# Performance work log

Measured on AMD Instinct MI355X. Metric: run time of the kernel, lower is better.

## Reference

```python
import jax, jax.numpy as jnp
import numpy as np

DIM = 192
HEADS = 6
HD = DIM // HEADS          # head dim = 32
WIN = 7
K = WIN * WIN              # 49 window positions
B, H, W = 4, 56, 56
EPS = 1e-5                 # BatchNorm2d eps
PAD = WIN // 2


def setup_inputs() -> dict:
    key = jax.random.key(0)
    ks = jax.random.split(key, 8)
    def n(k, shape, scale=0.02):
        return jax.random.normal(k, shape, dtype=jnp.float32) * scale
    return {
        "x": jax.random.normal(ks[0], (B, DIM, H, W), dtype=jnp.float32),
        "bn_gamma": jnp.ones((DIM,), jnp.float32),
        "bn_beta": jnp.zeros((DIM,), jnp.float32),
        "qkv_w": n(ks[1], (3 * DIM, DIM)),          # 1x1 conv as matmul
        "qkv_b": jnp.zeros((3 * DIM,), jnp.float32),
        "dm_w": n(ks[2], (K, 2 * HD, WIN, WIN)),    # convDotMul OIHW
        "dm_b": jnp.zeros((K,), jnp.float32),
        "rel_bias": n(ks[3], (K, HEADS)),           # relative_position_bias_table
        "proj_w": n(ks[4], (DIM, DIM)),
        "proj_b": jnp.zeros((DIM,), jnp.float32),
        "c1_w": n(ks[5], (4 * DIM, DIM)),
        "c1_b": jnp.zeros((4 * DIM,), jnp.float32),
        "c2_w": n(ks[6], (DIM, 4 * DIM)),
        "c2_b": jnp.zeros((DIM,), jnp.float32),
    }


def _conv1x1(x, w, b):
    # x: (B,C,H,W), w: (O,C) -> (B,O,H,W)
    return jnp.einsum('bchw,oc->bohw', x, w) + b[None, :, None, None]


def reference(x, bn_gamma, bn_beta, qkv_w, qkv_b, dm_w, dm_b, rel_bias,
              proj_w, proj_b, c1_w, c1_b, c2_w, c2_b):
    Bx, C, Hx, Wx = x.shape
    shortcut = x
    # BatchNorm2d (training-mode batch statistics, biased variance)
    mean = jnp.mean(x, axis=(0, 2, 3), keepdims=True)
    var = jnp.var(x, axis=(0, 2, 3), keepdims=True)
    xn = (x - mean) * jax.lax.rsqrt(var + EPS)
    xn = xn * bn_gamma[None, :, None, None] + bn_beta[None, :, None, None]
    # qkv: 1x1 conv -> (B,3,heads,hd,H,W)
    qkv = _conv1x1(xn, qkv_w, qkv_b).reshape(Bx, 3, HEADS, HD, Hx, Wx)
    q, k, v = qkv[:, 0], qkv[:, 1], qkv[:, 2]
    scale = HD ** (-0.5)
    # convDotMul on concat(q*scale, k) over merged (B*heads) batch
    qk = jnp.concatenate([(q * scale).reshape(Bx * HEADS, HD, Hx, Wx),
                          k.reshape(Bx * HEADS, HD, Hx, Wx)], axis=1)
    attn = jax.lax.conv_general_dilated(
        qk, dm_w, (1, 1), [(PAD, PAD), (PAD, PAD)],
        dimension_numbers=('NCHW', 'OIHW', 'NCHW')) + dm_b[None, :, None, None]
    attn = attn.reshape(Bx, HEADS, K, Hx, Wx)
    attn = attn + rel_bias.T[None, :, :, None, None]   # (1,heads,K,1,1)
    attn = jax.nn.softmax(attn, axis=2)
    # gather 49 zero-padded shifted views of v via patch extraction
    # channels of patches are (hd, kh*kw) row-major == torch loop i//7, i%7
    patches = jax.lax.conv_general_dilated_patches(
        v.reshape(Bx * HEADS, HD, Hx, Wx), (WIN, WIN), (1, 1),
        [(PAD, PAD), (PAD, PAD)], dimension_numbers=('NCHW', 'OIHW', 'NCHW'))
    patches = patches.reshape(Bx, HEADS, HD, K, Hx, Wx)
    out = jnp.einsum('bnckhw,bnkhw->bnchw', patches, attn).reshape(Bx, C, Hx, Wx)
    out = _conv1x1(out, proj_w, proj_b)
    x1 = shortcut + out
    # convLayers MLP (1x1 convs, exact GELU)
    h = _conv1x1(x1, c1_w, c1_b)
    h = jax.nn.gelu(h, approximate=False)
    h = _conv1x1(h, c2_w, c2_b)
    return x1 + h
```

## Files before the change

### kernel.cpp

```cpp
#include <hip/hip_runtime.h>
#include <hip/hip_bf16.h>
#include <math.h>

#define CDIM 192
#define NHEADS 6
#define WIN 7
#define KWIN 49
#define BATCH 4
#define PIX 3136
#define NPIX 12544
#define NIMG 24
#define EPSV 1e-5f

typedef __bf16 bf16x8 __attribute__((ext_vector_type(8)));
typedef float f32x16 __attribute__((ext_vector_type(16)));
typedef unsigned int uint4v __attribute__((ext_vector_type(4)));
typedef unsigned int uint2v __attribute__((ext_vector_type(2)));
typedef int int4x __attribute__((ext_vector_type(4)));
typedef int int8x __attribute__((ext_vector_type(8)));
typedef unsigned short u16;
typedef unsigned char u8;

__device__ inline u8 f32_to_fp8(float v) {
  return (u8)(__builtin_amdgcn_cvt_pk_fp8_f32(v, 0.f, 0, false) & 0xFF);
}

__device__ inline uint2v bf8_to_fp8x8(uint4v v) {
  const u16* h = (const u16*)&v;
  float f[8];
#pragma unroll
  for (int e = 0; e < 8; e++) {
    unsigned u = ((unsigned)h[e]) << 16;
    f[e] = __builtin_bit_cast(float, u);
  }
  int lo = __builtin_amdgcn_cvt_pk_fp8_f32(f[0], f[1], 0, false);
  lo = __builtin_amdgcn_cvt_pk_fp8_f32(f[2], f[3], lo, true);
  int hi = __builtin_amdgcn_cvt_pk_fp8_f32(f[4], f[5], 0, false);
  hi = __builtin_amdgcn_cvt_pk_fp8_f32(f[6], f[7], hi, true);
  uint2v r = {(unsigned)lo, (unsigned)hi};
  return r;
}

__global__ __launch_bounds__(256) void bn_stats_k(const float* __restrict__ x,
                                                  float* __restrict__ stats) {
  int c = blockIdx.x;
  float s = 0.f, q = 0.f;
  for (int n = threadIdx.x; n < BATCH * PIX; n += 256) {
    int b = n / PIX, p = n - b * PIX;
    float v = x[((size_t)b * CDIM + c) * PIX + p];
    s += v; q += v * v;
  }
  __shared__ float rs[256], rq[256];
  rs[threadIdx.x] = s; rq[threadIdx.x] = q;
  __syncthreads();
  for (int st = 128; st > 0; st >>= 1) {
    if (threadIdx.x < st) { rs[threadIdx.x] += rs[threadIdx.x + st]; rq[threadIdx.x] += rq[threadIdx.x + st]; }
    __syncthreads();
  }
  if (threadIdx.x == 0) {
    float mean = rs[0] / (float)(BATCH * PIX);
    float var = rq[0] / (float)(BATCH * PIX) - mean * mean;
    stats[c] = mean;
    stats[CDIM + c] = rsqrtf(var + EPSV);
  }
}

__device__ inline void pack_one(const float* __restrict__ W, u16* __restrict__ out,
                                int Cin, int t) {
  int lane = t & 63, rest = t >> 6;
  int nK = Cin >> 4;
  int kk = rest % nK, mtg = rest / nK;
  int o = mtg * 32 + (lane & 31), c = kk * 16 + (lane >> 5) * 8;
  const float* src = W + (size_t)o * Cin + c;
  __hip_bfloat16 tmp[8];
#pragma unroll
  for (int e = 0; e < 8; e++) tmp[e] = __float2bfloat16(src[e]);
  *(uint4v*)(out + (size_t)t * 8) = *(uint4v*)tmp;
}

__global__ __launch_bounds__(256) void prep4_k(
    const float* __restrict__ qkv_w, const float* __restrict__ qkv_b,
    const float* __restrict__ gamma, const float* __restrict__ beta,
    const float* __restrict__ stats, u16* __restrict__ pk_qkv,
    float* __restrict__ b_eff,
    const float* __restrict__ dm_w, u8* __restrict__ wTs8,
    const float* __restrict__ proj_w, u16* __restrict__ pk_proj,
    const float* __restrict__ c1_w, u16* __restrict__ pk_c1,
    const float* __restrict__ c2_w, u16* __restrict__ pk_c2) {
  __shared__ float r[CDIM];
  int bid = blockIdx.x, tid = threadIdx.x;
  if (bid < 576) {
    int o = bid;
    if (tid < CDIM) {
      int c = tid;
      float alpha = gamma[c] * stats[CDIM + c];
      float shift = beta[c] - stats[c] * alpha;
      float w = qkv_w[o * CDIM + c];
      float scale = (o < CDIM) ? 0.17677669529663687f : 1.f;
      int t8 = ((((o >> 5) * 12 + (c >> 4)) * 64 + (((c >> 3) & 1) * 32 + (o & 31))) << 3) + (c & 7);
      ((__hip_bfloat16*)pk_qkv)[t8] = __float2bfloat16(w * alpha * scale);
      r[c] = w * shift;
    }
    __syncthreads();
    if (tid == 0) {
      float s = 0.f;
      for (int i = 0; i < CDIM; i++) s += r[i];
      float scale = (o < CDIM) ? 0.17677669529663687f : 1.f;
      b_eff[o] = (qkv_b[o] + s) * scale;
    }
  } else if (bid < 1360) {
    int idx = (bid - 576) * 256 + tid;
    int e = idx & 31;
    int tmp = idx >> 5;
    int lane = tmp & 63; tmp >>= 6;
    int Mt = tmp & 1;
    int tap = tmp >> 1;
    int ko = Mt * 32 + (lane & 31);
    int ci = (lane >> 5) * 32 + e;
    float v = (ko < KWIN) ? dm_w[(size_t)ko * 3136 + ci * 49 + tap] : 0.f;
    wTs8[idx] = f32_to_fp8(v);
  } else if (bid < 1378) {
    int t = (bid - 1360) * 256 + tid;
    if (t < 4608) pack_one(proj_w, pk_proj, 192, t);
  } else if (bid < 1450) {
    int t = (bid - 1378) * 256 + tid;
    if (t < 18432) pack_one(c1_w, pk_c1, 192, t);
  } else {
    int t = (bid - 1450) * 256 + tid;
    if (t < 18432) pack_one(c2_w, pk_c2, 768, t);
  }
}

#define MG_QKV 0
#define MG_PROJ 1
#define MG_GELU 2
#define MG_C2 3
#define MG2S 1032

template <int EPI>
__global__ __launch_bounds__(256, 3) void mgemm_k(
    const u16* __restrict__ Bm, const u16* __restrict__ Apk,
    const float* __restrict__ bias,
    float* __restrict__ outF, u16* __restrict__ outT, u16* __restrict__ outT2,
    u8* __restrict__ outQK8,
    const float* __restrict__ extra, int Cin) {
  __shared__ __align__(16) u16 Bs[2][8 * MG2S];
  __shared__ __align__(16) u16 As[2][4096];
  int tid = threadIdx.x;
  int lane = tid & 63, wid = tid >> 6;
  int hi = lane >> 5, ln31 = lane & 31;
  int p0 = blockIdx.x * 128;
  int o0 = blockIdx.y * 64;
  int nK = Cin >> 4;
  int nKC = Cin >> 6;
  f32x16 acc[2];
#pragma unroll
  for (int mt = 0; mt < 2; mt++)
#pragma unroll
    for (int i = 0; i < 16; i++) acc[mt][i] = 0.f;

  uint4v bReg[4], aReg[2];

  auto loadC = [&](int kc) {
    int cc = kc * 64;
    if (EPI == MG_QKV) {
      int px = tid & 127, gh = tid >> 7;
      unsigned gp = p0 + px;
      unsigned bb = gp / PIX, pp = gp - bb * PIX;
#pragma unroll
      for (int j = 0; j < 4; j++) {
        int g = gh * 4 + j;
        const float* xb = extra + ((size_t)bb * CDIM + cc + g * 8) * PIX + pp;
        __hip_bfloat16 t8[8];
#pragma unroll
        for (int e = 0; e < 8; e++) t8[e] = __float2bfloat16(xb[(size_t)e * PIX]);
        bReg[j] = *(uint4v*)t8;
      }
    } else {
#pragma unroll
      for (int i = 0; i < 4; i++) {
        int idx = i * 256 + tid;
        int px = idx >> 3, g = idx & 7;
        bReg[i] = *(const uint4v*)(Bm + (size_t)(p0 + px) * Cin + cc + g * 8);
      }
    }
#pragma unroll
    for (int i = 0; i < 2; i++) {
      int idx = i * 256 + tid;
      int frag = idx >> 6, l64 = idx & 63;
      int mt = frag >> 2, ks = frag & 3;
      aReg[i] = *(const uint4v*)(Apk +
          (size_t)(((o0 >> 5) + mt) * nK + kc * 4 + ks) * 512 + l64 * 8);
    }
  };
  auto storeC = [&](int buf) {
    if (EPI == MG_QKV) {
      int px = tid & 127, gh = tid >> 7;
#pragma unroll
      for (int j = 0; j < 4; j++)
        *(uint4v*)&Bs[buf][(gh * 4 + j) * MG2S + px * 8] = bReg[j];
    } else {
#pragma unroll
      for (int i = 0; i < 4; i++) {
        int idx = i * 256 + tid;
        int px = idx >> 3, g = idx & 7;
        *(uint4v*)&Bs[buf][g * MG2S + px * 8] = bReg[i];
      }
    }
#pragma unroll
    for (int i = 0; i < 2; i++) {
      int idx = i * 256 + tid;
      int frag = idx >> 6, l64 = idx & 63;
      *(uint4v*)&As[buf][frag * 512 + l64 * 8] = aReg[i];
    }
  };

  loadC(0);
  storeC(0);
  __syncthreads();
  int pxw = wid * 32 + ln31;
  for (int kc = 0; kc < nKC; kc++) {
    int cur = kc & 1;
    bool more = (kc + 1 < nKC);
    if (more) loadC(kc + 1);
#pragma unroll
    for (int ks = 0; ks < 4; ks++) {
      int g = ks * 2 + hi;
      bf16x8 b  = *(const bf16x8*)&Bs[cur][g * MG2S + pxw * 8];
      bf16x8 a0 = *(const bf16x8*)&As[cur][ks * 512 + lane * 8];
      bf16x8 a1 = *(const bf16x8*)&As[cur][(4 + ks) * 512 + lane * 8];
      acc[0] = __builtin_amdgcn_mfma_f32_32x32x16_bf16(a0, b, acc[0], 0, 0, 0);
      acc[1] = __builtin_amdgcn_mfma_f32_32x32x16_bf16(a1, b, acc[1], 0, 0, 0);
    }
    if (more) storeC(cur ^ 1);
    __syncthreads();
  }

  if (EPI == MG_C2) {
#pragma unroll
    for (int mt = 0; mt < 2; mt++)
#pragma unroll
      for (int r = 0; r < 16; r++) {
        int o = o0 + mt * 32 + (r & 3) + 8 * (r >> 2) + 4 * hi;
        float bv = bias[o];
        unsigned gp = p0 + pxw;
        unsigned bb = gp / PIX, pp = gp - bb * PIX;
        size_t oi = ((size_t)bb * CDIM + o) * PIX + pp;
        outF[oi] = acc[mt][r] + bv + extra[oi];
      }
  } else {
    u16* scratch = (u16*)Bs;
#pragma unroll
    for (int mt = 0; mt < 2; mt++)
#pragma unroll
      for (int r = 0; r < 16; r++) {
        int o_loc = mt * 32 + (r & 3) + 8 * (r >> 2) + 4 * hi;
        int o = o0 + o_loc;
        float bv = bias[o];
        int p_loc = pxw;
        float val = acc[mt][r] + bv;
        if (EPI == MG_PROJ) {
          unsigned gp = p0 + p_loc;
          unsigned bb = gp / PIX, pp = gp - bb * PIX;
          size_t oi = ((size_t)bb * CDIM + o) * PIX + pp;
          val += extra[oi];
          outF[oi] = val;
        }
        if (EPI == MG_GELU)
          val = 0.5f * val * (1.f + erff(val * 0.70710678118654752f));
        *(__hip_bfloat16*)&scratch[p_loc * 64 + (((o_loc >> 3) ^ (p_loc & 7)) << 3) + (o_loc & 7)] =
            __float2bfloat16(val);
      }
    __syncthreads();
    int prow = tid >> 1, half = tid & 1;
    int psw = prow & 7;
    uint4v r4[4];
#pragma unroll
    for (int j = 0; j < 4; j++)
      r4[j] = *(const uint4v*)&scratch[prow * 64 + ((((half << 2) + j) ^ psw) << 3)];
    unsigned gp = p0 + prow;
    if (EPI == MG_QKV) {
      unsigned bb = gp / PIX, pp = gp - bb * PIX;
      int s = o0 / 192;
      int h0 = ((o0 - s * 192) >> 5) + half;
      if (s < 2) {
        uint2v c0 = bf8_to_fp8x8(r4[0]), c1 = bf8_to_fp8x8(r4[1]);
        uint2v c2 = bf8_to_fp8x8(r4[2]), c3 = bf8_to_fp8x8(r4[3]);
        uint4v w0 = {c0[0], c0[1], c1[0], c1[1]};
        uint4v w1 = {c2[0], c2[1], c3[0], c3[1]};
        u8* d = outQK8 + ((size_t)(bb * NHEADS + h0) * PIX + pp) * 64 + s * 32;
        *(uint4v*)(d) = w0; *(uint4v*)(d + 16) = w1;
      } else {
        u16* d = outT2 + ((size_t)(bb * NHEADS + h0) * PIX + pp) * 32;
        *(uint4v*)(d) = r4[0]; *(uint4v*)(d + 8) = r4[1];
        *(uint4v*)(d + 16) = r4[2]; *(uint4v*)(d + 24) = r4[3];
      }
    } else if (EPI == MG_PROJ) {
      u16* d = outT + (size_t)gp * CDIM + o0 + half * 32;
#pragma unroll
      for (int j = 0; j < 4; j++) *(uint4v*)(d + j * 8) = r4[j];
    } else {
      u16* d = outT + (size_t)gp * 768 + o0 + half * 32;
#pragma unroll
      for (int j = 0; j < 4; j++) *(uint4v*)(d + j * 8) = r4[j];
    }
  }
}

#define VPS 40
#define SMS 65
#define DIV7(t) (((t) * 9363) >> 16)
#define LPOF(t) ((t) + 7 * DIV7(t))

__global__ __launch_bounds__(256, 5) void attn_fused_k(
    const u8* __restrict__ qk8, const u8* __restrict__ wTs8,
    const u16* __restrict__ vT,
    const float* __restrict__ dm_b, const float* __restrict__ rel_bias,
    u16* __restrict__ attnoT) {
  __shared__ __align__(16) u16 shraw[14216];
  u8* patchB = (u8*)shraw;
  int img = blockIdx.x / 49;
  int tile = blockIdx.x % 49;
  int y0 = (tile / 7) * 8, x0 = (tile % 7) * 8;
  int tid = threadIdx.x;
  const u8* qimg = qk8 + (size_t)img * PIX * 64;
  for (int idx = tid; idx < 784; idx += 256) {
    int lp = idx >> 2, slot = idx & 3;
    int r = lp / 14, c = lp - r * 14;
    int gy = y0 - 3 + r, gx = x0 - 3 + c;
    uint4v val = {0u, 0u, 0u, 0u};
    if ((unsigned)gy < 56u && (unsigned)gx < 56u)
      val = *(const uint4v*)(qimg + (size_t)(gy * 56 + gx) * 64 + slot * 16);
    *(uint4v*)&patchB[lp * 64 + ((slot ^ ((lp >> 1) & 3)) << 4)] = val;
  }
  __syncthreads();

  const u16* vbase = vT + (size_t)img * PIX * 32;
  uint4v vreg[4];
#pragma unroll
  for (int s = 0; s < 4; s++) {
    int idx = s * 256 + tid;
    uint4v val = {0u, 0u, 0u, 0u};
    if (s < 3 || idx < 784) {
      int g = idx & 3, lp = idx >> 2;
      int r = lp / 14, c = lp - r * 14;
      int gy = y0 - 3 + r, gx = x0 - 3 + c;
      if ((unsigned)gy < 56u && (unsigned)gx < 56u)
        val = *(const uint4v*)(vbase + (size_t)(gy * 56 + gx) * 32 + g * 8);
    }
    vreg[s] = val;
  }

  int lane = tid & 63, wid = tid >> 6;
  int Mtile = wid & 1, Ntile = wid >> 1;
  int n = lane & 31, hi = lane >> 5;
  int py = Ntile * 4 + (n >> 3), px = n & 7;
  int lpb = py * 14 + px;
  f32x16 acc0, acc1;
#pragma unroll
  for (int i = 0; i < 16; i++) { acc0[i] = 0.f; acc1[i] = 0.f; }

  const u8* Aw = wTs8 + Mtile * 2048 + lane * 32;
#pragma unroll
  for (int tap = 0; tap < KWIN; tap++) {
    int lp_ = lpb + LPOF(tap);
    const int4x* ap = (const int4x*)(Aw + tap * 4096);
    int4x alo = ap[0], ahi = ap[1];
    int sw = (lp_ >> 1) & 3;
    int4x blo = *(const int4x*)&patchB[lp_ * 64 + (((2 * hi) ^ sw) << 4)];
    int4x bhi = *(const int4x*)&patchB[lp_ * 64 + (((2 * hi + 1) ^ sw) << 4)];
    int8x a = __builtin_shufflevector(alo, ahi, 0, 1, 2, 3, 4, 5, 6, 7);
    int8x b = __builtin_shufflevector(blo, bhi, 0, 1, 2, 3, 4, 5, 6, 7);
    if (tap & 1)
      acc1 = __builtin_amdgcn_mfma_scale_f32_32x32x64_f8f6f4(
          a, b, acc1, 0, 0, 0, 127, 0, 127);
    else
      acc0 = __builtin_amdgcn_mfma_scale_f32_32x32x64_f8f6f4(
          a, b, acc0, 0, 0, 0, 127, 0, 127);
  }

  __syncthreads();
  float* smx = (float*)shraw;
  u16* vp = shraw + 6376;
  int head = img % NHEADS;
#pragma unroll
  for (int r = 0; r < 16; r++) {
    int ko = Mtile * 32 + (r & 3) + 8 * (r >> 2) + 4 * hi;
    if (ko < KWIN)
      smx[ko * SMS + Ntile * 32 + n] =
          acc0[r] + acc1[r] + dm_b[ko] + rel_bias[ko * NHEADS + head];
  }
#pragma unroll
  for (int s = 0; s < 4; s++) {
    int idx = s * 256 + tid;
    if (s < 3 || idx < 784) {
      int g = idx & 3, lp = idx >> 2;
      *(uint4v*)&vp[lp * VPS + g * 8] = vreg[s];
    }
  }
  __syncthreads();
  {
    int pxs = tid >> 2, q4 = tid & 3;
    int k0 = q4 * 13;
    int k1 = (q4 == 3) ? KWIN : k0 + 13;
    float m = -1e30f;
    for (int k = k0; k < k1; k++) m = fmaxf(m, smx[k * SMS + pxs]);
    m = fmaxf(m, __shfl_xor(m, 1, 64));
    m = fmaxf(m, __shfl_xor(m, 2, 64));
    float ssum = 0.f;
    for (int k = k0; k < k1; k++) {
      float e = __expf(smx[k * SMS + pxs] - m);
      smx[k * SMS + pxs] = e;
      ssum += e;
    }
    ssum += __shfl_xor(ssum, 1, 64);
    ssum += __shfl_xor(ssum, 2, 64);
    float inv = 1.f / ssum;
    for (int k = k0; k < k1; k++) smx[k * SMS + pxs] *= inv;
  }
  __syncthreads();
  int pxl = tid & 63, co = tid >> 6;
  int pyy = pxl >> 3, pxx = pxl & 7;
  float o8[8] = {0.f, 0.f, 0.f, 0.f, 0.f, 0.f, 0.f, 0.f};
#pragma unroll
  for (int kh = 0; kh < 7; kh++) {
#pragma unroll
    for (int kw = 0; kw < 7; kw++) {
      float p = smx[(kh * 7 + kw) * SMS + pxl];
      bf16x8 v = *(const bf16x8*)&vp[((pyy + kh) * 14 + pxx + kw) * VPS + co * 8];
#pragma unroll
      for (int j = 0; j < 8; j++) o8[j] += p * (float)v[j];
    }
  }
  int gp = (y0 + pyy) * 56 + x0 + pxx;
  int b = img / NHEADS;
  __hip_bfloat16 ob[8];
#pragma unroll
  for (int j = 0; j < 8; j++) ob[j] = __float2bfloat16(o8[j]);
  *(uint4v*)(attnoT + ((size_t)b * PIX + gp) * CDIM + head * 32 + co * 8) = *(uint4v*)ob;
}

extern "C" void kernel_launch(void* const* d_in, const int* in_sizes, int n_in,
                              void* d_out, int out_size, void* d_ws, size_t ws_size,
                              hipStream_t stream) {
  const float* x        = (const float*)d_in[0];
  const float* bn_gamma = (const float*)d_in[1];
  const float* bn_beta  = (const float*)d_in[2];
  const float* qkv_w    = (const float*)d_in[3];
  const float* qkv_b    = (const float*)d_in[4];
  const float* dm_w     = (const float*)d_in[5];
  const float* dm_b     = (const float*)d_in[6];
  const float* rel_bias = (const float*)d_in[7];
  const float* proj_w   = (const float*)d_in[8];
  const float* proj_b   = (const float*)d_in[9];
  const float* c1_w     = (const float*)d_in[10];
  const float* c1_b     = (const float*)d_in[11];
  const float* c2_w     = (const float*)d_in[12];
  const float* c2_b     = (const float*)d_in[13];
  float* out = (float*)d_out;
  float* ws  = (float*)d_ws;

  float* stats   = ws;
  float* b_eff   = stats + 384;
  u16*   pk_qkv  = (u16*)(b_eff + 576);
  u16*   pk_proj = pk_qkv + 110592;
  u16*   pk_c1   = pk_proj + 36864;
  u16*   pk_c2   = pk_c1 + 147456;
  u8*    wTs8    = (u8*)(pk_c2 + 147456);
  u16*   spare   = (u16*)(wTs8 + 200704);
  u8*    qk8     = (u8*)(spare + 4816896);
  u16*   vT      = (u16*)(qk8 + 4816896);
  u16*   attnoT  = vT + 2408448;
  float* x1      = (float*)(attnoT + 2408448);
  u16*   x1T     = (u16*)(x1 + 2408448);
  u16*   hT      = spare;

  bn_stats_k<<<CDIM, 256, 0, stream>>>(x, stats);
  prep4_k<<<1522, 256, 0, stream>>>(qkv_w, qkv_b, bn_gamma, bn_beta, stats,
                                    pk_qkv, b_eff, dm_w, wTs8,
                                    proj_w, pk_proj, c1_w, pk_c1, c2_w, pk_c2);

  mgemm_k<MG_QKV><<<dim3(98, 9), 256, 0, stream>>>(
      nullptr, pk_qkv, b_eff, nullptr, nullptr, vT, qk8, x, 192);
  attn_fused_k<<<NIMG * 49, 256, 0, stream>>>(qk8, wTs8, vT, dm_b, rel_bias, attnoT);
  mgemm_k<MG_PROJ><<<dim3(98, 3), 256, 0, stream>>>(
      attnoT, pk_proj, proj_b, x1, x1T, nullptr, nullptr, x, 192);
  mgemm_k<MG_GELU><<<dim3(98, 12), 256, 0, stream>>>(
      x1T, pk_c1, c1_b, nullptr, hT, nullptr, nullptr, nullptr, 192);
  mgemm_k<MG_C2><<<dim3(98, 3), 256, 0, stream>>>(
      hT, pk_c2, c2_b, out, nullptr, nullptr, nullptr, x1, 768);
}
```

Measured before the change: 117.6 us.

## Switch all 1x1-conv GEMMs to FP8 MFMA with FP8 activations

```diff
diff --git a/kernel.cpp b/kernel.cpp
--- a/kernel.cpp
+++ b/kernel.cpp
@@ -41,6 +41,15 @@
   return r;
 }
 
+__device__ inline uint2v f32x8_to_fp8(const float* f) {
+  int lo = __builtin_amdgcn_cvt_pk_fp8_f32(f[0], f[1], 0, false);
+  lo = __builtin_amdgcn_cvt_pk_fp8_f32(f[2], f[3], lo, true);
+  int hi = __builtin_amdgcn_cvt_pk_fp8_f32(f[4], f[5], 0, false);
+  hi = __builtin_amdgcn_cvt_pk_fp8_f32(f[6], f[7], hi, true);
+  uint2v r = {(unsigned)lo, (unsigned)hi};
+  return r;
+}
+
 __global__ __launch_bounds__(256) void bn_stats_k(const float* __restrict__ x,
                                                   float* __restrict__ stats) {
   int c = blockIdx.x;
@@ -65,40 +74,44 @@
   }
 }
 
-__device__ inline void pack_one(const float* __restrict__ W, u16* __restrict__ out,
-                                int Cin, int t) {
+__device__ inline void pack8_one(const float* __restrict__ W, u8* __restrict__ out,
+                                 int Cin, int t, int total) {
+  if (t >= total) return;
   int lane = t & 63, rest = t >> 6;
-  int nK = Cin >> 4;
-  int kk = rest % nK, mtg = rest / nK;
-  int o = mtg * 32 + (lane & 31), c = kk * 16 + (lane >> 5) * 8;
+  int nKC = Cin >> 6;
+  int kc = rest % nKC, oT = rest / nKC;
+  int o = oT * 32 + (lane & 31), c = kc * 64 + (lane >> 5) * 32;
   const float* src = W + (size_t)o * Cin + c;
-  __hip_bfloat16 tmp[8];
-#pragma unroll
-  for (int e = 0; e < 8; e++) tmp[e] = __float2bfloat16(src[e]);
-  *(uint4v*)(out + (size_t)t * 8) = *(uint4v*)tmp;
-}
-
-__global__ __launch_bounds__(256) void prep4_k(
+  u8 tmp[32];
+#pragma unroll
+  for (int e = 0; e < 32; e++) tmp[e] = f32_to_fp8(src[e]);
+  *(uint4v*)(out + (size_t)t * 32) = *(uint4v*)tmp;
+  *(uint4v*)(out + (size_t)t * 32 + 16) = *(uint4v*)(tmp + 16);
+}
+
+__global__ __launch_bounds__(256) void prep5_k(
     const float* __restrict__ qkv_w, const float* __restrict__ qkv_b,
     const float* __restrict__ gamma, const float* __restrict__ beta,
-    const float* __restrict__ stats, u16* __restrict__ pk_qkv,
+    const float* __restrict__ stats, u8* __restrict__ pk_qkv8,
     float* __restrict__ b_eff,
     const float* __restrict__ dm_w, u8* __restrict__ wTs8,
-    const float* __restrict__ proj_w, u16* __restrict__ pk_proj,
-    const float* __restrict__ c1_w, u16* __restrict__ pk_c1,
-    const float* __restrict__ c2_w, u16* __restrict__ pk_c2) {
-  __shared__ float r[CDIM];
+    const float* __restrict__ proj_w, u8* __restrict__ pk_proj8,
+    const float* __restrict__ c1_w, u8* __restrict__ pk_c18,
+    const float* __restrict__ c2_w, u8* __restrict__ pk_c28,
+    const float* __restrict__ x, u8* __restrict__ xT8) {
+  __shared__ float shf[64 * 33];
   int bid = blockIdx.x, tid = threadIdx.x;
   if (bid < 576) {
     int o = bid;
+    float* r = shf;
     if (tid < CDIM) {
       int c = tid;
       float alpha = gamma[c] * stats[CDIM + c];
       float shift = beta[c] - stats[c] * alpha;
       float w = qkv_w[o * CDIM + c];
       float scale = (o < CDIM) ? 0.17677669529663687f : 1.f;
-      int t8 = ((((o >> 5) * 12 + (c >> 4)) * 64 + (((c >> 3) & 1) * 32 + (o & 31))) << 3) + (c & 7);
-      ((__hip_bfloat16*)pk_qkv)[t8] = __float2bfloat16(w * alpha * scale);
+      int bidx = (((o >> 5) * 3 + (c >> 6)) * 64 + (((c >> 5) & 1) * 32 + (o & 31))) * 32 + (c & 31);
+      pk_qkv8[bidx] = f32_to_fp8(w * alpha * scale);
       r[c] = w * shift;
     }
     __syncthreads();
@@ -119,15 +132,32 @@
     int ci = (lane >> 5) * 32 + e;
     float v = (ko < KWIN) ? dm_w[(size_t)ko * 3136 + ci * 49 + tap] : 0.f;
     wTs8[idx] = f32_to_fp8(v);
-  } else if (bid < 1378) {
-    int t = (bid - 1360) * 256 + tid;
-    if (t < 4608) pack_one(proj_w, pk_proj, 192, t);
-  } else if (bid < 1450) {
-    int t = (bid - 1378) * 256 + tid;
-    if (t < 18432) pack_one(c1_w, pk_c1, 192, t);
+  } else if (bid < 1365) {
+    pack8_one(proj_w, pk_proj8, 192, (bid - 1360) * 256 + tid, 1152);
+  } else if (bid < 1383) {
+    pack8_one(c1_w, pk_c18, 192, (bid - 1365) * 256 + tid, 4608);
+  } else if (bid < 1401) {
+    pack8_one(c2_w, pk_c28, 768, (bid - 1383) * 256 + tid, 4608);
   } else {
-    int t = (bid - 1450) * 256 + tid;
-    if (t < 18432) pack_one(c2_w, pk_c2, 768, t);
+    int t = bid - 1401;
+    int bx = t % 196, by = t / 196;
+    int bb = bx / 49;
+    int p0 = (bx % 49) * 64;
+    int c0 = by * 32;
+    float (*Ls)[33] = (float(*)[33])shf;
+    int j = tid & 63;
+#pragma unroll
+    for (int it = 0; it < 8; it++) {
+      int c = it * 4 + (tid >> 6);
+      Ls[j][c] = x[((size_t)bb * CDIM + c0 + c) * PIX + p0 + j];
+    }
+    __syncthreads();
+    int jr = tid >> 2, tt = tid & 3;
+    float f[8];
+#pragma unroll
+    for (int u = 0; u < 8; u++) f[u] = Ls[jr][tt * 8 + u];
+    uint2v w = f32x8_to_fp8(f);
+    *(uint2v*)(xT8 + (size_t)(bb * PIX + p0 + jr) * CDIM + c0 + tt * 8) = w;
   }
 }
 
@@ -135,23 +165,21 @@
 #define MG_PROJ 1
 #define MG_GELU 2
 #define MG_C2 3
-#define MG2S 1032
 
 template <int EPI>
-__global__ __launch_bounds__(256, 3) void mgemm_k(
-    const u16* __restrict__ Bm, const u16* __restrict__ Apk,
+__global__ __launch_bounds__(256, 4) void mgemm8_k(
+    const u8* __restrict__ Bm8, const u8* __restrict__ Apk8,
     const float* __restrict__ bias,
-    float* __restrict__ outF, u16* __restrict__ outT, u16* __restrict__ outT2,
+    float* __restrict__ outF, u8* __restrict__ outT8, u16* __restrict__ outT2,
     u8* __restrict__ outQK8,
     const float* __restrict__ extra, int Cin) {
-  __shared__ __align__(16) u16 Bs[2][8 * MG2S];
-  __shared__ __align__(16) u16 As[2][4096];
+  __shared__ __align__(16) u8 Bs8[2][8192];
+  __shared__ __align__(16) u8 As8[2][4096];
   int tid = threadIdx.x;
   int lane = tid & 63, wid = tid >> 6;
   int hi = lane >> 5, ln31 = lane & 31;
   int p0 = blockIdx.x * 128;
   int o0 = blockIdx.y * 64;
-  int nK = Cin >> 4;
   int nKC = Cin >> 6;
   f32x16 acc[2];
 #pragma unroll
@@ -159,79 +187,51 @@
 #pragma unroll
     for (int i = 0; i < 16; i++) acc[mt][i] = 0.f;
 
-  uint4v bReg[4], aReg[2];
-
+  uint4v bReg[2], aReg;
   auto loadC = [&](int kc) {
     int cc = kc * 64;
-    if (EPI == MG_QKV) {
-      int px = tid & 127, gh = tid >> 7;
-      unsigned gp = p0 + px;
-      unsigned bb = gp / PIX, pp = gp - bb * PIX;
-#pragma unroll
-      for (int j = 0; j < 4; j++) {
-        int g = gh * 4 + j;
-        const float* xb = extra + ((size_t)bb * CDIM + cc + g * 8) * PIX + pp;
-        __hip_bfloat16 t8[8];
-#pragma unroll
-        for (int e = 0; e < 8; e++) t8[e] = __float2bfloat16(xb[(size_t)e * PIX]);
-        bReg[j] = *(uint4v*)t8;
-      }
-    } else {
-#pragma unroll
-      for (int i = 0; i < 4; i++) {
-        int idx = i * 256 + tid;
-        int px = idx >> 3, g = idx & 7;
-        bReg[i] = *(const uint4v*)(Bm + (size_t)(p0 + px) * Cin + cc + g * 8);
-      }
-    }
 #pragma unroll
     for (int i = 0; i < 2; i++) {
       int idx = i * 256 + tid;
-      int frag = idx >> 6, l64 = idx & 63;
-      int mt = frag >> 2, ks = frag & 3;
-      aReg[i] = *(const uint4v*)(Apk +
-          (size_t)(((o0 >> 5) + mt) * nK + kc * 4 + ks) * 512 + l64 * 8);
-    }
+      int px = idx >> 2, slot = idx & 3;
+      bReg[i] = *(const uint4v*)(Bm8 + (size_t)(p0 + px) * Cin + cc + slot * 16);
+    }
+    int frag = tid >> 7, off = (tid & 127) * 16;
+    aReg = *(const uint4v*)(Apk8 + (size_t)(((o0 >> 5) + frag) * nKC + kc) * 2048 + off);
   };
   auto storeC = [&](int buf) {
-    if (EPI == MG_QKV) {
-      int px = tid & 127, gh = tid >> 7;
-#pragma unroll
-      for (int j = 0; j < 4; j++)
-        *(uint4v*)&Bs[buf][(gh * 4 + j) * MG2S + px * 8] = bReg[j];
-    } else {
-#pragma unroll
-      for (int i = 0; i < 4; i++) {
-        int idx = i * 256 + tid;
-        int px = idx >> 3, g = idx & 7;
-        *(uint4v*)&Bs[buf][g * MG2S + px * 8] = bReg[i];
-      }
-    }
 #pragma unroll
     for (int i = 0; i < 2; i++) {
       int idx = i * 256 + tid;
-      int frag = idx >> 6, l64 = idx & 63;
-      *(uint4v*)&As[buf][frag * 512 + l64 * 8] = aReg[i];
-    }
+      int px = idx >> 2, slot = idx & 3;
+      *(uint4v*)&Bs8[buf][px * 64 + ((slot ^ (px & 3)) << 4)] = bReg[i];
+    }
+    int frag = tid >> 7, off = (tid & 127) * 16;
+    *(uint4v*)&As8[buf][frag * 2048 + off] = aReg;
   };
 
   loadC(0);
   storeC(0);
   __syncthreads();
   int pxw = wid * 32 + ln31;
+  int swb = pxw & 3;
   for (int kc = 0; kc < nKC; kc++) {
     int cur = kc & 1;
     bool more = (kc + 1 < nKC);
     if (more) loadC(kc + 1);
-#pragma unroll
-    for (int ks = 0; ks < 4; ks++) {
-      int g = ks * 2 + hi;
-      bf16x8 b  = *(const bf16x8*)&Bs[cur][g * MG2S + pxw * 8];
-      bf16x8 a0 = *(const bf16x8*)&As[cur][ks * 512 + lane * 8];
-      bf16x8 a1 = *(const bf16x8*)&As[cur][(4 + ks) * 512 + lane * 8];
-      acc[0] = __builtin_amdgcn_mfma_f32_32x32x16_bf16(a0, b, acc[0], 0, 0, 0);
-      acc[1] = __builtin_amdgcn_mfma_f32_32x32x16_bf16(a1, b, acc[1], 0, 0, 0);
-    }
+    int4x a0lo = *(const int4x*)&As8[cur][lane * 32];
+    int4x a0hi = *(const int4x*)&As8[cur][lane * 32 + 16];
+    int4x a1lo = *(const int4x*)&As8[cur][2048 + lane * 32];
+    int4x a1hi = *(const int4x*)&As8[cur][2048 + lane * 32 + 16];
+    int4x blo = *(const int4x*)&Bs8[cur][pxw * 64 + (((2 * hi) ^ swb) << 4)];
+    int4x bhi = *(const int4x*)&Bs8[cur][pxw * 64 + (((2 * hi + 1) ^ swb) << 4)];
+    int8x a0 = __builtin_shufflevector(a0lo, a0hi, 0, 1, 2, 3, 4, 5, 6, 7);
+    int8x a1 = __builtin_shufflevector(a1lo, a1hi, 0, 1, 2, 3, 4, 5, 6, 7);
+    int8x b = __builtin_shufflevector(blo, bhi, 0, 1, 2, 3, 4, 5, 6, 7);
+    acc[0] = __builtin_amdgcn_mfma_scale_f32_32x32x64_f8f6f4(
+        a0, b, acc[0], 0, 0, 0, 127, 0, 127);
+    acc[1] = __builtin_amdgcn_mfma_scale_f32_32x32x64_f8f6f4(
+        a1, b, acc[1], 0, 0, 0, 127, 0, 127);
     if (more) storeC(cur ^ 1);
     __syncthreads();
   }
@@ -249,7 +249,7 @@
         outF[oi] = acc[mt][r] + bv + extra[oi];
       }
   } else {
-    u16* scratch = (u16*)Bs;
+    u16* scratch = (u16*)Bs8;
 #pragma unroll
     for (int mt = 0; mt < 2; mt++)
 #pragma unroll
@@ -295,14 +295,14 @@
         *(uint4v*)(d) = r4[0]; *(uint4v*)(d + 8) = r4[1];
         *(uint4v*)(d + 16) = r4[2]; *(uint4v*)(d + 24) = r4[3];
       }
-    } else if (EPI == MG_PROJ) {
-      u16* d = outT + (size_t)gp * CDIM + o0 + half * 32;
-#pragma unroll
-      for (int j = 0; j < 4; j++) *(uint4v*)(d + j * 8) = r4[j];
     } else {
-      u16* d = outT + (size_t)gp * 768 + o0 + half * 32;
-#pragma unroll
-      for (int j = 0; j < 4; j++) *(uint4v*)(d + j * 8) = r4[j];
+      uint2v c0 = bf8_to_fp8x8(r4[0]), c1 = bf8_to_fp8x8(r4[1]);
+      uint2v c2 = bf8_to_fp8x8(r4[2]), c3 = bf8_to_fp8x8(r4[3]);
+      uint4v w0 = {c0[0], c0[1], c1[0], c1[1]};
+      uint4v w1 = {c2[0], c2[1], c3[0], c3[1]};
+      int stride = (EPI == MG_PROJ) ? CDIM : 768;
+      u8* d = outT8 + (size_t)gp * stride + o0 + half * 32;
+      *(uint4v*)(d) = w0; *(uint4v*)(d + 16) = w1;
     }
   }
 }
@@ -316,7 +316,7 @@
     const u8* __restrict__ qk8, const u8* __restrict__ wTs8,
     const u16* __restrict__ vT,
     const float* __restrict__ dm_b, const float* __restrict__ rel_bias,
-    u16* __restrict__ attnoT) {
+    u8* __restrict__ attnoT8) {
   __shared__ __align__(16) u16 shraw[14216];
   u8* patchB = (u8*)shraw;
   int img = blockIdx.x / 49;
@@ -434,10 +434,8 @@
   }
   int gp = (y0 + pyy) * 56 + x0 + pxx;
   int b = img / NHEADS;
-  __hip_bfloat16 ob[8];
-#pragma unroll
-  for (int j = 0; j < 8; j++) ob[j] = __float2bfloat16(o8[j]);
-  *(uint4v*)(attnoT + ((size_t)b * PIX + gp) * CDIM + head * 32 + co * 8) = *(uint4v*)ob;
+  uint2v w = f32x8_to_fp8(o8);
+  *(uint2v*)(attnoT8 + ((size_t)b * PIX + gp) * CDIM + head * 32 + co * 8) = w;
 }
 
 extern "C" void kernel_launch(void* const* d_in, const int* in_sizes, int n_in,
@@ -460,33 +458,34 @@
   float* out = (float*)d_out;
   float* ws  = (float*)d_ws;
 
-  float* stats   = ws;
-  float* b_eff   = stats + 384;
-  u16*   pk_qkv  = (u16*)(b_eff + 576);
-  u16*   pk_proj = pk_qkv + 110592;
-  u16*   pk_c1   = pk_proj + 36864;
-  u16*   pk_c2   = pk_c1 + 147456;
-  u8*    wTs8    = (u8*)(pk_c2 + 147456);
-  u16*   spare   = (u16*)(wTs8 + 200704);
-  u8*    qk8     = (u8*)(spare + 4816896);
-  u16*   vT      = (u16*)(qk8 + 4816896);
-  u16*   attnoT  = vT + 2408448;
-  float* x1      = (float*)(attnoT + 2408448);
-  u16*   x1T     = (u16*)(x1 + 2408448);
-  u16*   hT      = spare;
+  float* stats    = ws;
+  float* b_eff    = stats + 384;
+  u8*    pk_qkv8  = (u8*)(b_eff + 576);
+  u8*    pk_proj8 = pk_qkv8 + 110592;
+  u8*    pk_c18   = pk_proj8 + 36864;
+  u8*    pk_c28   = pk_c18 + 147456;
+  u8*    wTs8     = pk_c28 + 147456;
+  u8*    xT8      = wTs8 + 200704;
+  u8*    qk8      = xT8 + 2408448;
+  u16*   vT       = (u16*)(qk8 + 4816896);
+  u8*    attnoT8  = (u8*)(vT + 2408448);
+  float* x1       = (float*)(attnoT8 + 2408448);
+  u8*    x1T8     = (u8*)(x1 + 2408448);
+  u8*    hT8      = x1T8 + 2408448;
 
   bn_stats_k<<<CDIM, 256, 0, stream>>>(x, stats);
-  prep4_k<<<1522, 256, 0, stream>>>(qkv_w, qkv_b, bn_gamma, bn_beta, stats,
-                                    pk_qkv, b_eff, dm_w, wTs8,
-                                    proj_w, pk_proj, c1_w, pk_c1, c2_w, pk_c2);
-
-  mgemm_k<MG_QKV><<<dim3(98, 9), 256, 0, stream>>>(
-      nullptr, pk_qkv, b_eff, nullptr, nullptr, vT, qk8, x, 192);
-  attn_fused_k<<<NIMG * 49, 256, 0, stream>>>(qk8, wTs8, vT, dm_b, rel_bias, attnoT);
-  mgemm_k<MG_PROJ><<<dim3(98, 3), 256, 0, stream>>>(
-      attnoT, pk_proj, proj_b, x1, x1T, nullptr, nullptr, x, 192);
-  mgemm_k<MG_GELU><<<dim3(98, 12), 256, 0, stream>>>(
-      x1T, pk_c1, c1_b, nullptr, hT, nullptr, nullptr, nullptr, 192);
-  mgemm_k<MG_C2><<<dim3(98, 3), 256, 0, stream>>>(
-      hT, pk_c2, c2_b, out, nullptr, nullptr, nullptr, x1, 768);
-}
+  prep5_k<<<2577, 256, 0, stream>>>(qkv_w, qkv_b, bn_gamma, bn_beta, stats,
+                                    pk_qkv8, b_eff, dm_w, wTs8,
+                                    proj_w, pk_proj8, c1_w, pk_c18,
+                                    c2_w, pk_c28, x, xT8);
+
+  mgemm8_k<MG_QKV><<<dim3(98, 9), 256, 0, stream>>>(
+      xT8, pk_qkv8, b_eff, nullptr, nullptr, vT, qk8, nullptr, 192);
+  attn_fused_k<<<NIMG * 49, 256, 0, stream>>>(qk8, wTs8, vT, dm_b, rel_bias, attnoT8);
+  mgemm8_k<MG_PROJ><<<dim3(98, 3), 256, 0, stream>>>(
+      attnoT8, pk_proj8, proj_b, x1, x1T8, nullptr, nullptr, x, 192);
+  mgemm8_k<MG_GELU><<<dim3(98, 12), 256, 0, stream>>>(
+      x1T8, pk_c18, c1_b, nullptr, hT8, nullptr, nullptr, nullptr, 192);
+  mgemm8_k<MG_C2><<<dim3(98, 3), 256, 0, stream>>>(
+      hT8, pk_c28, c2_b, out, nullptr, nullptr, nullptr, x1, 768);
+}
```

Result: faster. 97.95 us (-16.7%).
